# Kernel optimization log

Hardware: AMD Instinct MI355X
Metric: run time of the kernel (lower is better)

The kernel has to match this reference:

```python
import jax, jax.numpy as jnp
import numpy as np

LMAX = 2
C1 = 64; C2 = 64; COUT = 64
B = 4096
SUM_RDIM = sum(3**L for L in range(LMAX + 1))   # 13
FEAT1 = C1 * SUM_RDIM                            # 832
FEAT2 = C2 * SUM_RDIM


def _enumerate_paths(Lmax):
    paths = []
    for L1 in range(Lmax + 1):
        for L2 in range(Lmax + 1):
            for k in range(min(L1, L2) + 1):
                Lout = L1 + L2 - 2 * k
                if 0 <= Lout <= Lmax:
                    paths.append((L1, L2, Lout, k, False))
            if L1 >= 1 and L2 >= 1:
                for k in range(min(L1 - 1, L2 - 1) + 1):
                    Lout = L1 + L2 - 2 * k - 1
                    if 0 <= Lout <= Lmax:
                        paths.append((L1, L2, Lout, k, True))
    return paths

PATHS = _enumerate_paths(LMAX)   # 15 paths for Lmax=2


def _path_eq(L1, L2, k, use_eps):
    # Fused equation: W[c,a,b] contracted together with the delta/eps path einsum.
    letters = list('defghijklmnopqrstuvwxyz')  # a,b,c reserved for channels
    i_idx = letters[:L1]
    j_idx = letters[L1:L1 + L2]
    for r in range(k):  # delta: contract last k indices of A with last k of B
        j_idx[L2 - k + r] = i_idx[L1 - k + r]
    i_free = i_idx[:L1 - k]
    j_free = j_idx[:L2 - k]
    eps_sub = None
    if use_eps:  # consume last free index of each side via eps_{p i j}
        p = letters[L1 + L2]
        eps_sub = p + i_free[-1] + j_free[-1]
        i_free, j_free = i_free[:-1], j_free[:-1]
        out = i_free + j_free + [p]
    else:
        out = i_free + j_free
    terms = ['cab', '...a' + ''.join(i_idx), '...b' + ''.join(j_idx)]
    if eps_sub is not None:
        terms.append(eps_sub)
    return ','.join(terms) + '->...c' + ''.join(out)


def _epsilon():
    e = np.zeros((3, 3, 3), dtype=np.float32)
    e[0, 1, 2] = e[1, 2, 0] = e[2, 0, 1] = 1.0
    e[2, 1, 0] = e[1, 0, 2] = e[0, 2, 1] = -1.0
    return jnp.asarray(e)


def _split_by_rank(x, C, Lmax):
    batch = x.shape[:-1]
    out, idx = {}, 0
    for L in range(Lmax + 1):
        d = C * 3**L
        blk = x[..., idx:idx + d]
        idx += d
        out[L] = blk.reshape(*batch, C) if L == 0 else blk.reshape(*batch, C, *((3,) * L))
    return out


def setup_inputs() -> dict:
    key = jax.random.key(0)
    k1, k2, k3 = jax.random.split(key, 3)
    x1 = jax.random.normal(k1, (B, FEAT1), dtype=jnp.float32)
    x2 = jax.random.normal(k2, (B, FEAT2), dtype=jnp.float32)
    weight = jax.random.normal(k3, (len(PATHS) * COUT * C1 * C2,), dtype=jnp.float32) * 0.02
    return {"x1": x1, "x2": x2, "weight": weight}


def reference(x1, x2, weight):
    A = _split_by_rank(x1, C1, LMAX)
    Bt = _split_by_rank(x2, C2, LMAX)
    eps = _epsilon().astype(x1.dtype)
    batch = x1.shape[:-1]
    blocks = {L: jnp.zeros((*batch, COUT) + (3,) * L, dtype=x1.dtype) for L in range(LMAX + 1)}
    wsz = COUT * C1 * C2
    for n, (L1, L2, Lout, k, use_eps) in enumerate(PATHS):
        Wp = weight[n * wsz:(n + 1) * wsz].reshape(COUT, C1, C2)
        eq = _path_eq(L1, L2, k, use_eps)
        ops = (Wp, A[L1], Bt[L2]) + ((eps,) if use_eps else ())
        blocks[Lout] = blocks[Lout] + jnp.einsum(eq, *ops, optimize='optimal')
    parts = [blocks[L].reshape(*batch, COUT * 3**L) for L in range(LMAX + 1)]
    return jnp.concatenate(parts, axis=-1)
```

## Files before the change

kernel.cpp:

```cpp
#include <hip/hip_runtime.h>
#include <cstdint>
#include <cstddef>


#define FEAT 832
#define ZT 64

typedef _Float16 half8 __attribute__((ext_vector_type(8)));
typedef float floatx16 __attribute__((ext_vector_type(16)));

struct Chunk {
  int wbase;
  int o1[3];
  int o2[3];
  float sg[3];
  int d1, d2, nt;
};

__global__ void swz_w_kernel(const float* __restrict__ w, _Float16* __restrict__ o) {
  const int i = blockIdx.x * 256 + threadIdx.x;
  const int lane = i & 63;
  const int pkc  = i >> 6;
  const int cgrp = pkc & 1;
  const int ksg  = (pkc >> 1) & 255;
  const int p    = pkc >> 9;
  const int c  = cgrp * 32 + (lane & 31);
  const int k0 = ksg * 16 + (lane >> 5) * 8;
  const float* src = w + (size_t)p * 262144 + (size_t)c * 4096 + k0;
  const float4 v0 = *(const float4*)(src);
  const float4 v1 = *(const float4*)(src + 4);
  half8 h = { (_Float16)v0.x, (_Float16)v0.y, (_Float16)v0.z, (_Float16)v0.w,
              (_Float16)v1.x, (_Float16)v1.y, (_Float16)v1.z, (_Float16)v1.w };
  *(half8*)(o + (size_t)i * 8) = h;
}

__device__ __forceinline__ half8 splat8(_Float16 h) {
  return half8{h, h, h, h, h, h, h, h};
}

template<int NT>
__device__ __forceinline__ void run_chunk(
    const Chunk C, const int zbase, const int zl, const int hf,
    const int lane, const int tid,
    const float* __restrict__ x1, const float* __restrict__ x2,
    const _Float16* __restrict__ Wh, _Float16* __restrict__ XS1,
    floatx16& acc0, floatx16& acc1)
{
  half8 x2r[NT][4];
  {
    const float* __restrict__ x2z = x2 + (size_t)(zbase + zl) * FEAT;
    #pragma unroll
    for (int t = 0; t < NT; ++t) {
      const float* __restrict__ p = x2z + C.o2[t];
      #pragma unroll
      for (int ks = 0; ks < 4; ++ks) {
        const int b0 = ks * 16 + hf * 8;
        half8 h;
        #pragma unroll
        for (int j = 0; j < 8; ++j) h[j] = (_Float16)p[(b0 + j) * C.d2];
        x2r[t][ks] = h;
      }
    }
  }

  __syncthreads();

  #pragma unroll
  for (int t = 0; t < NT; ++t) {
    const float sgf = C.sg[t];
    const int o1 = C.o1[t];
    for (int e = tid; e < 4096; e += 128) {
      const int a = e & 63, zz = e >> 6;
      XS1[(t * 64 + a) * 66 + zz] =
          (_Float16)(x1[(size_t)(zbase + zz) * FEAT + o1 + a * C.d1] * sgf);
    }
  }
  __syncthreads();

  const _Float16* __restrict__ Wq = Wh + C.wbase + lane * 8;
  const _Float16* __restrict__ Xq = XS1 + zl;

  half8 afE[2][4], afO[2][4];
  #pragma unroll
  for (int ks = 0; ks < 4; ++ks) {
    afE[0][ks] = *(const half8*)(Wq + ks * 1024);
    afE[1][ks] = *(const half8*)(Wq + ks * 1024 + 512);
    afO[0][ks] = *(const half8*)(Wq + 4096 + ks * 1024);
    afO[1][ks] = *(const half8*)(Wq + 4096 + ks * 1024 + 512);
  }
  _Float16 sc[NT], scn[NT];
  #pragma unroll
  for (int t = 0; t < NT; ++t) {
    sc[t]  = Xq[(t * 64 + 0) * 66];
    scn[t] = Xq[(t * 64 + 1) * 66];
  }

  #pragma unroll 1
  for (int a = 0; a < 64; a += 2) {
    {
      half8 sv[NT];
      #pragma unroll
      for (int t = 0; t < NT; ++t) sv[t] = splat8(sc[t]);
      if (a + 2 < 64) {
        #pragma unroll
        for (int t = 0; t < NT; ++t) sc[t] = Xq[(t * 64 + a + 2) * 66];
      }
      #pragma unroll
      for (int ks = 0; ks < 4; ++ks) {
        half8 tb = sv[0] * x2r[0][ks];
        if (NT > 1) tb += sv[1] * x2r[1][ks];
        if (NT > 2) tb += sv[2] * x2r[2][ks];
        acc0 = __builtin_amdgcn_mfma_f32_32x32x16_f16(afE[0][ks], tb, acc0, 0, 0, 0);
        acc1 = __builtin_amdgcn_mfma_f32_32x32x16_f16(afE[1][ks], tb, acc1, 0, 0, 0);
      }
      if (a + 2 < 64) {
        const _Float16* wn = Wq + (a + 2) * 4096;
        #pragma unroll
        for (int ks = 0; ks < 4; ++ks) {
          afE[0][ks] = *(const half8*)(wn + ks * 1024);
          afE[1][ks] = *(const half8*)(wn + ks * 1024 + 512);
        }
      }
    }
    {
      half8 sv[NT];
      #pragma unroll
      for (int t = 0; t < NT; ++t) sv[t] = splat8(scn[t]);
      if (a + 3 < 64) {
        #pragma unroll
        for (int t = 0; t < NT; ++t) scn[t] = Xq[(t * 64 + a + 3) * 66];
      }
      #pragma unroll
      for (int ks = 0; ks < 4; ++ks) {
        half8 tb = sv[0] * x2r[0][ks];
        if (NT > 1) tb += sv[1] * x2r[1][ks];
        if (NT > 2) tb += sv[2] * x2r[2][ks];
        acc0 = __builtin_amdgcn_mfma_f32_32x32x16_f16(afO[0][ks], tb, acc0, 0, 0, 0);
        acc1 = __builtin_amdgcn_mfma_f32_32x32x16_f16(afO[1][ks], tb, acc1, 0, 0, 0);
      }
      if (a + 3 < 64) {
        const _Float16* wn = Wq + (a + 3) * 4096;
        #pragma unroll
        for (int ks = 0; ks < 4; ++ks) {
          afO[0][ks] = *(const half8*)(wn + ks * 1024);
          afO[1][ks] = *(const half8*)(wn + ks * 1024 + 512);
        }
      }
    }
  }
}

__global__ __launch_bounds__(128, 2) void tp_kernel(
    const float* __restrict__ x1, const float* __restrict__ x2,
    const _Float16* __restrict__ Wh, float* __restrict__ out)
{
  __shared__ __align__(16) _Float16 XS1[3 * 64 * 66];
  __shared__ Chunk chs[7];
  __shared__ int nch_s;

  const int tid  = threadIdx.x;
  const int slot = blockIdx.y;
  const int zbase = blockIdx.x * ZT;
  const int zgrp = tid >> 6;
  const int lane = tid & 63;
  const int ln31 = lane & 31;
  const int hf   = lane >> 5;
  const int zl   = zgrp * 32 + ln31;

  int offO, dO, mO;
  if (slot == 0)      { offO = 0;   dO = 1; mO = 0; }
  else if (slot < 4)  { offO = 64;  dO = 3; mO = slot - 1; }
  else                { offO = 256; dO = 9; mO = slot - 4; }

  if (tid == 0) {
    int n = 0;
    auto add = [&](int p, int L1, int L2,
                   int i0, int i1, int i2, int j0, int j1, int j2,
                   float s0, float s1, float s2, int nt) {
      const int offs[3] = {0, 64, 256};
      const int ds[3]   = {1, 3, 9};
      Chunk c;
      c.wbase = p * 262144;
      c.o1[0] = offs[L1] + i0; c.o1[1] = offs[L1] + i1; c.o1[2] = offs[L1] + i2;
      c.o2[0] = offs[L2] + j0; c.o2[1] = offs[L2] + j1; c.o2[2] = offs[L2] + j2;
      c.sg[0] = s0; c.sg[1] = s1; c.sg[2] = s2;
      c.d1 = ds[L1]; c.d2 = ds[L2]; c.nt = nt;
      chs[n++] = c;
    };
    if (slot == 0) {
      add(0, 0,0, 0,0,0, 0,0,0, 1,0,0, 1);
      add(5, 1,1, 0,1,2, 0,1,2, 1,1,1, 3);
      add(13,2,2, 0,1,2, 0,1,2, 1,1,1, 3);
      add(13,2,2, 3,4,5, 3,4,5, 1,1,1, 3);
      add(13,2,2, 6,7,8, 6,7,8, 1,1,1, 3);
    } else if (slot < 4) {
      const int m = slot - 1, p1 = (m+1)%3, p2 = (m+2)%3;
      add(1, 0,1, 0,0,0, m,0,0, 1,0,0, 1);
      add(3, 1,0, m,0,0, 0,0,0, 1,0,0, 1);
      add(6, 1,1, p1,p2,0, p2,p1,0, 1,-1,0, 2);
      add(7, 1,2, 0,1,2, 3*m,3*m+1,3*m+2, 1,1,1, 3);
      add(10,2,1, 3*m,3*m+1,3*m+2, 0,1,2, 1,1,1, 3);
      add(14,2,2, 3*p1,3*p1+1,3*p1+2, 3*p2,3*p2+1,3*p2+2, 1,1,1, 3);
      add(14,2,2, 3*p2,3*p2+1,3*p2+2, 3*p1,3*p1+1,3*p1+2, -1,-1,-1, 3);
    } else {
      const int m = slot - 4, u = m/3, v = m%3, q1 = (v+1)%3, q2 = (v+2)%3;
      add(2, 0,2, 0,0,0, m,0,0, 1,0,0, 1);
      add(4, 1,1, u,0,0, v,0,0, 1,0,0, 1);
      add(8, 1,2, q1,q2,0, 3*u+q2,3*u+q1,0, 1,-1,0, 2);
      add(9, 2,0, m,0,0, 0,0,0, 1,0,0, 1);
      add(11,2,1, 3*u+q1,3*u+q2,0, q2,q1,0, 1,-1,0, 2);
      add(12,2,2, 3*u,3*u+1,3*u+2, 3*v,3*v+1,3*v+2, 1,1,1, 3);
    }
    nch_s = n;
  }
  __syncthreads();
  const int nch = nch_s;

  floatx16 acc0, acc1;
  #pragma unroll
  for (int r = 0; r < 16; ++r) { acc0[r] = 0.0f; acc1[r] = 0.0f; }

  for (int ci = 0; ci < nch; ++ci) {
    const Chunk C = chs[ci];
    if (C.nt == 1)      run_chunk<1>(C, zbase, zl, hf, lane, tid, x1, x2, Wh, XS1, acc0, acc1);
    else if (C.nt == 2) run_chunk<2>(C, zbase, zl, hf, lane, tid, x1, x2, Wh, XS1, acc0, acc1);
    else                run_chunk<3>(C, zbase, zl, hf, lane, tid, x1, x2, Wh, XS1, acc0, acc1);
  }

  float* __restrict__ op = out + (size_t)(zbase + zl) * FEAT + offO + mO;
  #pragma unroll
  for (int r = 0; r < 16; ++r) {
    const int cr = (r & 3) + 8 * (r >> 2) + 4 * hf;
    op[(size_t)cr * dO]        = acc0[r];
    op[(size_t)(cr + 32) * dO] = acc1[r];
  }
}

extern "C" void kernel_launch(void* const* d_in, const int* in_sizes, int n_in,
                              void* d_out, int out_size, void* d_ws, size_t ws_size,
                              hipStream_t stream) {
  const float* x1 = (const float*)d_in[0];
  const float* x2 = (const float*)d_in[1];
  const float* w  = (const float*)d_in[2];
  float* out = (float*)d_out;
  _Float16* Wh = (_Float16*)d_ws;

  const int nchunks = 15 * 64 * 4096 / 8;
  hipLaunchKernelGGL(swz_w_kernel, dim3(nchunks / 256), dim3(256), 0, stream, w, Wh);

  dim3 grid(64, 13);
  hipLaunchKernelGGL(tp_kernel, grid, dim3(128), 0, stream, x1, x2, Wh, out);
}
```

Baseline: 408.1 us.

## Split chunk loop across two blocks with atomic output accumulation

Result: slower. 772.3 us (+89.2%).

```diff
diff --git a/kernel.cpp b/kernel.cpp
--- a/kernel.cpp
+++ b/kernel.cpp
@@ -34,6 +34,11 @@
   *(half8*)(o + (size_t)i * 8) = h;
 }
 
+__global__ void zero_out_kernel(float4* __restrict__ o, int n4) {
+  const int i = blockIdx.x * 256 + threadIdx.x;
+  if (i < n4) o[i] = float4{0.f, 0.f, 0.f, 0.f};
+}
+
 __device__ __forceinline__ half8 splat8(_Float16 h) {
   return half8{h, h, h, h, h, h, h, h};
 }
@@ -43,26 +48,29 @@
     const Chunk C, const int zbase, const int zl, const int hf,
     const int lane, const int tid,
     const float* __restrict__ x1, const float* __restrict__ x2,
-    const _Float16* __restrict__ Wh, _Float16* __restrict__ XS1,
+    const _Float16* __restrict__ Wh, _Float16* __restrict__ XS,
     floatx16& acc0, floatx16& acc1)
 {
+  __syncthreads();
+
+  #pragma unroll
+  for (int t = 0; t < NT; ++t) {
+    const size_t base2 = (size_t)zbase * FEAT + C.o2[t];
+    for (int e = tid; e < 4096; e += 128) {
+      const int zz = e >> 6, b = e & 63;
+      XS[(t * 64 + zz) * 72 + b] =
+          (_Float16)x2[base2 + (size_t)zz * FEAT + b * C.d2];
+    }
+  }
+  __syncthreads();
+
   half8 x2r[NT][4];
-  {
-    const float* __restrict__ x2z = x2 + (size_t)(zbase + zl) * FEAT;
+  #pragma unroll
+  for (int t = 0; t < NT; ++t) {
     #pragma unroll
-    for (int t = 0; t < NT; ++t) {
-      const float* __restrict__ p = x2z + C.o2[t];
-      #pragma unroll
-      for (int ks = 0; ks < 4; ++ks) {
-        const int b0 = ks * 16 + hf * 8;
-        half8 h;
-        #pragma unroll
-        for (int j = 0; j < 8; ++j) h[j] = (_Float16)p[(b0 + j) * C.d2];
-        x2r[t][ks] = h;
-      }
-    }
-  }
-
+    for (int ks = 0; ks < 4; ++ks)
+      x2r[t][ks] = *(const half8*)&XS[(t * 64 + zl) * 72 + ks * 16 + hf * 8];
+  }
   __syncthreads();
 
   #pragma unroll
@@ -71,14 +79,14 @@
     const int o1 = C.o1[t];
     for (int e = tid; e < 4096; e += 128) {
       const int a = e & 63, zz = e >> 6;
-      XS1[(t * 64 + a) * 66 + zz] =
+      XS[(t * 64 + a) * 66 + zz] =
           (_Float16)(x1[(size_t)(zbase + zz) * FEAT + o1 + a * C.d1] * sgf);
     }
   }
   __syncthreads();
 
   const _Float16* __restrict__ Wq = Wh + C.wbase + lane * 8;
-  const _Float16* __restrict__ Xq = XS1 + zl;
+  const _Float16* __restrict__ Xq = XS + zl;
 
   half8 afE[2][4], afO[2][4];
   #pragma unroll
@@ -150,16 +158,17 @@
   }
 }
 
-__global__ __launch_bounds__(128, 2) void tp_kernel(
+__global__ __launch_bounds__(128, 3) void tp_kernel(
     const float* __restrict__ x1, const float* __restrict__ x2,
     const _Float16* __restrict__ Wh, float* __restrict__ out)
 {
-  __shared__ __align__(16) _Float16 XS1[3 * 64 * 66];
+  __shared__ __align__(16) _Float16 XS[3 * 64 * 72];
   __shared__ Chunk chs[7];
   __shared__ int nch_s;
 
   const int tid  = threadIdx.x;
   const int slot = blockIdx.y;
+  const int half = blockIdx.z;
   const int zbase = blockIdx.x * ZT;
   const int zgrp = tid >> 6;
   const int lane = tid & 63;
@@ -220,19 +229,19 @@
   #pragma unroll
   for (int r = 0; r < 16; ++r) { acc0[r] = 0.0f; acc1[r] = 0.0f; }
 
-  for (int ci = 0; ci < nch; ++ci) {
+  for (int ci = half; ci < nch; ci += 2) {
     const Chunk C = chs[ci];
-    if (C.nt == 1)      run_chunk<1>(C, zbase, zl, hf, lane, tid, x1, x2, Wh, XS1, acc0, acc1);
-    else if (C.nt == 2) run_chunk<2>(C, zbase, zl, hf, lane, tid, x1, x2, Wh, XS1, acc0, acc1);
-    else                run_chunk<3>(C, zbase, zl, hf, lane, tid, x1, x2, Wh, XS1, acc0, acc1);
+    if (C.nt == 1)      run_chunk<1>(C, zbase, zl, hf, lane, tid, x1, x2, Wh, XS, acc0, acc1);
+    else if (C.nt == 2) run_chunk<2>(C, zbase, zl, hf, lane, tid, x1, x2, Wh, XS, acc0, acc1);
+    else                run_chunk<3>(C, zbase, zl, hf, lane, tid, x1, x2, Wh, XS, acc0, acc1);
   }
 
   float* __restrict__ op = out + (size_t)(zbase + zl) * FEAT + offO + mO;
   #pragma unroll
   for (int r = 0; r < 16; ++r) {
     const int cr = (r & 3) + 8 * (r >> 2) + 4 * hf;
-    op[(size_t)cr * dO]        = acc0[r];
-    op[(size_t)(cr + 32) * dO] = acc1[r];
+    atomicAdd(op + (size_t)cr * dO,        acc0[r]);
+    atomicAdd(op + (size_t)(cr + 32) * dO, acc1[r]);
   }
 }
 
@@ -248,6 +257,10 @@
   const int nchunks = 15 * 64 * 4096 / 8;
   hipLaunchKernelGGL(swz_w_kernel, dim3(nchunks / 256), dim3(256), 0, stream, w, Wh);
 
-  dim3 grid(64, 13);
+  const int n4 = out_size / 4;
+  hipLaunchKernelGGL(zero_out_kernel, dim3((n4 + 255) / 256), dim3(256), 0, stream,
+                     (float4*)out, n4);
+
+  dim3 grid(64, 13, 2);
   hipLaunchKernelGGL(tp_kernel, grid, dim3(128), 0, stream, x1, x2, Wh, out);
 }
```
